# Performance work log

Measured on AMD Instinct MI355X. Metric: run time of the kernel, lower is better.

Reference implementation:

```python
import jax, jax.numpy as jnp
import numpy as np

MARGIN = 0.5
ALPHA = 1.0
BETA = 0.5
TEMP = 0.07
TEMP_MIN = 0.01
TEMP_MAX = 0.5
STEP = 1  # step_count after first forward (buffer starts at 0, incremented before use)
WARMUP = 1000


def _l2norm(x):
    return x / jnp.maximum(jnp.linalg.norm(x, axis=1, keepdims=True), 1e-12)


def _adaptive_temp(std):
    return jnp.clip(TEMP * (1.0 + std), TEMP_MIN, TEMP_MAX)


def setup_inputs() -> dict:
    key = jax.random.key(0)
    k1, k2, k3, k4, k5 = jax.random.split(key, 5)
    B, D, C, P = 4096, 1024, 1000, 2000
    return {
        "features": jax.random.normal(k1, (B, D), dtype=jnp.float32),
        "cur_proto": jax.random.normal(k2, (C, D), dtype=jnp.float32),
        "prev_proto": jax.random.normal(k3, (P, D), dtype=jnp.float32),
        "labels": jax.random.randint(k4, (B,), 0, C, dtype=jnp.int32),
        "prev_proto_labels": jax.random.randint(k5, (P,), 0, C, dtype=jnp.int32),
    }


def reference(features, cur_proto, prev_proto, labels, prev_proto_labels):
    # With randn protos, proto norms ~ sqrt(D)=32 in (1e-3, 100), so valid_mask
    # is all-True; the per-sample torch loop vectorizes exactly.
    f = _l2norm(features)          # [B, D]
    cp = _l2norm(cur_proto)        # [C, D]

    # --- positive alignment: cosine_embedding_loss(target=1) = mean(1 - cos) ---
    pos_cos = jnp.sum(f * cp[labels], axis=1)       # [B]
    pos_loss = jnp.mean(1.0 - pos_cos)

    # --- curriculum weight at step 1 ---
    w = 0.1 + 0.9 * (STEP / WARMUP)
    curr_beta = BETA * w

    # --- intra-domain InfoNCE vs current prototypes (smooth_loss branch) ---
    # all_sims per sample is a permutation of the full row of sims -> std invariant
    sims = f @ cp.T                                  # [B, C]
    std = jnp.std(sims, axis=1, ddof=1)              # torch.std is unbiased
    temp = _adaptive_temp(std)[:, None]              # [B, 1]
    logits = sims / temp
    pos_logit = jnp.take_along_axis(logits, labels[:, None], axis=1)[:, 0]
    infonce = jax.scipy.special.logsumexp(logits, axis=1) - pos_logit
    loss_neg_total = jnp.mean(infonce)

    # --- cross-domain vs previous-domain prototypes of different class ---
    pp = _l2norm(prev_proto)                         # [P, D]
    csims = f @ pp.T                                 # [B, P]
    m = (prev_proto_labels[None, :] != labels[:, None]).astype(f.dtype)  # [B, P]
    n = jnp.sum(m, axis=1)                           # [B], >1 w.h.p.
    mean = jnp.sum(csims * m, axis=1) / n
    var = jnp.sum(m * (csims - mean[:, None]) ** 2, axis=1) / (n - 1.0)
    ctemp = (_adaptive_temp(jnp.sqrt(var)) * 2.0)[:, None]
    clogits = jnp.where(m > 0, csims / ctemp, -jnp.inf)
    cross = jax.scipy.special.logsumexp(clogits, axis=1)  # [B]
    loss_neg_total = loss_neg_total + 0.3 * jnp.mean(cross)

    total = ALPHA * pos_loss + curr_beta * loss_neg_total
    return total
```

## Files before the change

kernel.cpp:

```cpp
#include <hip/hip_runtime.h>
#include <hip/hip_bf16.h>
#include <math.h>

typedef __attribute__((ext_vector_type(4))) float floatx4;
typedef __attribute__((ext_vector_type(8))) __bf16 bf16x8;

#define B_ROWS 4096
#define D_DIM  1024
#define C_CUR  1000
#define P_PREV 2000
#define C_PAD  1024
#define P_PAD  2048
#define N_TOT  (C_PAD + P_PAD)

#define LDS_BARRIER() asm volatile("s_waitcnt lgkmcnt(0)\n\ts_barrier" ::: "memory")

__device__ __forceinline__ float wave_sum(float v) {
#pragma unroll
  for (int o = 32; o > 0; o >>= 1) v += __shfl_xor(v, o, 64);
  return v;
}
__device__ __forceinline__ float wave_max(float v) {
#pragma unroll
  for (int o = 32; o > 0; o >>= 1) v = fmaxf(v, __shfl_xor(v, o, 64));
  return v;
}

__device__ __forceinline__ unsigned char f32_to_e4m3(float x) {
  unsigned u = __float_as_uint(x);
  unsigned s = (u >> 24) & 0x80u;
  float a = fabsf(x);
  if (a < 0.015625f) {
    int q = (int)rintf(a * 512.0f);
    return (unsigned char)(s | (unsigned)q);
  }
  unsigned au = u & 0x7fffffffu;
  unsigned r = au + 0x0007ffffu + ((au >> 20) & 1u);
  int e = (int)(r >> 23) - 127;
  unsigned m = (r >> 20) & 7u;
  return (unsigned char)(s | ((unsigned)(e + 7) << 3) | m);
}

__global__ __launch_bounds__(256) void norm_all_kernel(
    const float* __restrict__ features, const float* __restrict__ cur_proto,
    const float* __restrict__ prev_proto, unsigned char* __restrict__ fn,
    unsigned char* __restrict__ proto) {
  const int wv = threadIdx.x >> 6, lane = threadIdx.x & 63;
  const int r = blockIdx.x * 4 + wv;
  const float* src;
  unsigned char* dst;
  bool valid;
  if (r < B_ROWS) {
    src = features + (size_t)r * D_DIM;
    dst = fn + (size_t)r * D_DIM;
    valid = true;
  } else if (r < B_ROWS + C_PAD) {
    const int rr = r - B_ROWS;
    src = cur_proto + (size_t)rr * D_DIM;
    dst = proto + (size_t)rr * D_DIM;
    valid = rr < C_CUR;
  } else {
    const int rr = r - B_ROWS - C_PAD;
    src = prev_proto + (size_t)rr * D_DIM;
    dst = proto + (size_t)(C_PAD + rr) * D_DIM;
    valid = rr < P_PREV;
  }
  if (!valid) {
    uint4 z = {0, 0, 0, 0};
    *(uint4*)(dst + lane * 16) = z;
    return;
  }
  float4 v[4];
  float ss = 0.f;
#pragma unroll
  for (int k = 0; k < 4; ++k) {
    v[k] = *(const float4*)(src + lane * 16 + k * 4);
    ss += v[k].x * v[k].x + v[k].y * v[k].y + v[k].z * v[k].z + v[k].w * v[k].w;
  }
  ss = wave_sum(ss);
  const float inv = 1.0f / fmaxf(sqrtf(ss), 1e-12f);
  union { unsigned char b[16]; uint4 q; } o;
#pragma unroll
  for (int k = 0; k < 4; ++k) {
    o.b[k * 4 + 0] = f32_to_e4m3(v[k].x * inv);
    o.b[k * 4 + 1] = f32_to_e4m3(v[k].y * inv);
    o.b[k * 4 + 2] = f32_to_e4m3(v[k].z * inv);
    o.b[k * 4 + 3] = f32_to_e4m3(v[k].w * inv);
  }
  *(uint4*)(dst + lane * 16) = o.q;
}

#define TM    128
#define BK    32
#define LSTRB 48
#define KITER (D_DIM / BK)

__global__ __launch_bounds__(256) void gemm_fp8_kernel(
    const unsigned char* __restrict__ A,
    const unsigned char* __restrict__ Bm,
    __hip_bfloat16* __restrict__ Cm) {
  __shared__ alignas(16) unsigned char lA[2][TM * LSTRB];
  __shared__ alignas(16) unsigned char lB[2][TM * LSTRB];
  const int t = threadIdx.x;
  const int bm = blockIdx.y, bn = blockIdx.x;
  const unsigned char* Ag = A + (size_t)bm * TM * D_DIM;
  const unsigned char* Bg = Bm + (size_t)bn * TM * D_DIM;

  const int lane = t & 63, wv = t >> 6;
  const int wm = (wv >> 1) * 64, wn = (wv & 1) * 64;
  const int quad = lane >> 4, l16 = lane & 15;

  const int srow = t >> 1, shalf = (t & 1) * 16;
  const unsigned char* ap = Ag + (size_t)srow * D_DIM + shalf;
  const unsigned char* bp = Bg + (size_t)srow * D_DIM + shalf;
  const int wroff = srow * LSTRB + shalf;

  floatx4 acc[4][4] = {};

  float4 a0 = *(const float4*)(ap);
  float4 b0 = *(const float4*)(bp);
  *(float4*)(lA[0] + wroff) = a0;
  *(float4*)(lB[0] + wroff) = b0;
  a0 = *(const float4*)(ap + BK);
  b0 = *(const float4*)(bp + BK);
  LDS_BARRIER();

#pragma unroll 2
  for (int i = 0; i < KITER; ++i) {
    const int p = i & 1;
    if (i < KITER - 1) {
      *(float4*)(lA[1 - p] + wroff) = a0;
      *(float4*)(lB[1 - p] + wroff) = b0;
      const int nk = (i + 2 < KITER) ? (i + 2) * BK : (KITER - 1) * BK;
      a0 = *(const float4*)(ap + nk);
      b0 = *(const float4*)(bp + nk);
    }
    long long af[4], bfr[4];
#pragma unroll
    for (int x = 0; x < 4; ++x)
      af[x] = *(const long long*)(lA[p] + (wm + x * 16 + l16) * LSTRB + quad * 8);
#pragma unroll
    for (int y = 0; y < 4; ++y)
      bfr[y] = *(const long long*)(lB[p] + (wn + y * 16 + l16) * LSTRB + quad * 8);
#pragma unroll
    for (int x = 0; x < 4; ++x)
#pragma unroll
      for (int y = 0; y < 4; ++y)
        acc[x][y] = __builtin_amdgcn_mfma_f32_16x16x32_fp8_fp8(af[x], bfr[y], acc[x][y], 0, 0, 0);
    LDS_BARRIER();
  }

  unsigned short* Cu = (unsigned short*)Cm;
#pragma unroll
  for (int x = 0; x < 4; ++x)
#pragma unroll
    for (int y = 0; y < 4; ++y)
#pragma unroll
      for (int r = 0; r < 4; ++r) {
        const int row = bm * TM + wm + x * 16 + quad * 4 + r;
        const int col = bn * TM + wn + y * 16 + l16;
        __hip_bfloat16 h = __float2bfloat16(acc[x][y][r]);
        Cu[(size_t)row * N_TOT + col] = *(unsigned short*)&h;
      }
}

__global__ __launch_bounds__(256) void row_reduce_kernel(
    const __hip_bfloat16* __restrict__ sims, const int* __restrict__ labels,
    const int* __restrict__ ppl,
    float* __restrict__ pos_o, float* __restrict__ inf_o, float* __restrict__ crs_o) {
  const int wv = threadIdx.x >> 6, lane = threadIdx.x & 63;
  const int b = blockIdx.x * 4 + wv;
  const unsigned short* row = (const unsigned short*)sims + (size_t)b * N_TOT;
  const int lab = labels[b];

  {
    const int i1 = 512 + lane * 8;
    float vi[16];
    bf16x8 u0 = *(const bf16x8*)(row + lane * 8);
    bf16x8 u1 = *(const bf16x8*)(row + i1);
#pragma unroll
    for (int j = 0; j < 8; ++j) { vi[j] = (float)u0[j]; vi[8 + j] = (float)u1[j]; }
    float sum = 0.f, sq = 0.f, mx = -1e30f;
#pragma unroll
    for (int j = 0; j < 8; ++j) {
      float v = vi[j];
      sum += v; sq += v * v; mx = fmaxf(mx, v);
    }
#pragma unroll
    for (int j = 0; j < 8; ++j) {
      if (i1 + j < C_CUR) { float v = vi[8 + j]; sum += v; sq += v * v; mx = fmaxf(mx, v); }
    }
    sum = wave_sum(sum); sq = wave_sum(sq); mx = wave_max(mx);
    const float var = (sq - sum * sum / (float)C_CUR) / (float)(C_CUR - 1);
    const float sd = sqrtf(fmaxf(var, 0.f));
    const float temp = fminf(fmaxf(0.07f * (1.f + sd), 0.01f), 0.5f);
    const float it = 1.f / temp;
    float se = 0.f;
#pragma unroll
    for (int j = 0; j < 8; ++j) se += __expf((vi[j] - mx) * it);
#pragma unroll
    for (int j = 0; j < 8; ++j)
      if (i1 + j < C_CUR) se += __expf((vi[8 + j] - mx) * it);
    se = wave_sum(se);
    if (lane == 0) {
      __hip_bfloat16 hs;
      *(unsigned short*)&hs = row[lab];
      const float slab = __bfloat162float(hs);
      pos_o[b] = 1.f - slab;
      inf_o[b] = mx * it + logf(se) - slab * it;
    }
  }

  {
    const unsigned short* crow = row + C_PAD;
    float vc[32];
    unsigned mask = 0;
    float sum = 0.f, sq = 0.f, mx = -1e30f;
    int cnt = 0;
#pragma unroll
    for (int k = 0; k < 4; ++k) {
      const int base = k * 512 + lane * 8;
      bf16x8 u = *(const bf16x8*)(crow + base);
#pragma unroll
      for (int j = 0; j < 8; ++j) vc[k * 8 + j] = (float)u[j];
      if (base < P_PREV) {
        int4 p0 = *(const int4*)(ppl + base);
        int4 p1 = *(const int4*)(ppl + base + 4);
        const int pl[8] = {p0.x, p0.y, p0.z, p0.w, p1.x, p1.y, p1.z, p1.w};
#pragma unroll
        for (int j = 0; j < 8; ++j) {
          if (pl[j] != lab) {
            mask |= 1u << (k * 8 + j);
            float v = vc[k * 8 + j];
            sum += v; sq += v * v; mx = fmaxf(mx, v); ++cnt;
          }
        }
      }
    }
    sum = wave_sum(sum); sq = wave_sum(sq); mx = wave_max(mx);
    const float n = wave_sum((float)cnt);
    const float var = (sq - sum * sum / n) / (n - 1.f);
    const float sd = sqrtf(fmaxf(var, 0.f));
    const float ct = 2.f * fminf(fmaxf(0.07f * (1.f + sd), 0.01f), 0.5f);
    const float it = 1.f / ct;
    float se = 0.f;
#pragma unroll
    for (int e = 0; e < 32; ++e)
      if ((mask >> e) & 1u) se += __expf((vc[e] - mx) * it);
    se = wave_sum(se);
    if (lane == 0) crs_o[b] = mx * it + logf(se);
  }
}

__global__ __launch_bounds__(1024) void final_reduce_kernel(
    const float* __restrict__ pos_o, const float* __restrict__ inf_o,
    const float* __restrict__ crs_o, float* __restrict__ out) {
  const int t = threadIdx.x;
  __shared__ float sA[1024], sB[1024], sC[1024];
  float a = 0.f, bb = 0.f, c = 0.f;
  for (int i = t; i < B_ROWS; i += 1024) {
    a += pos_o[i]; bb += inf_o[i]; c += crs_o[i];
  }
  sA[t] = a; sB[t] = bb; sC[t] = c;
  __syncthreads();
  for (int o = 512; o > 0; o >>= 1) {
    if (t < o) { sA[t] += sA[t + o]; sB[t] += sB[t + o]; sC[t] += sC[t + o]; }
    __syncthreads();
  }
  if (t == 0) {
    const float invB = 1.f / (float)B_ROWS;
    const float pos = sA[0] * invB;
    const float neg = sB[0] * invB + 0.3f * sC[0] * invB;
    const float curr_beta = 0.5f * (0.1f + 0.9f * (1.0f / 1000.0f));
    out[0] = pos + curr_beta * neg;
  }
}

extern "C" void kernel_launch(void* const* d_in, const int* in_sizes, int n_in,
                              void* d_out, int out_size, void* d_ws, size_t ws_size,
                              hipStream_t stream) {
  const float* features   = (const float*)d_in[0];
  const float* cur_proto  = (const float*)d_in[1];
  const float* prev_proto = (const float*)d_in[2];
  const int*   labels     = (const int*)d_in[3];
  const int*   ppl        = (const int*)d_in[4];

  char* w = (char*)d_ws;
  unsigned char* fn    = (unsigned char*)w;
  unsigned char* proto = (unsigned char*)(w + (size_t)4 * 1024 * 1024);
  __hip_bfloat16* sims = (__hip_bfloat16*)(w + (size_t)8 * 1024 * 1024);
  char* tail = w + (size_t)8 * 1024 * 1024 + (size_t)B_ROWS * N_TOT * 2;
  float* pos_o = (float*)tail;
  float* inf_o = pos_o + B_ROWS;
  float* crs_o = inf_o + B_ROWS;

  norm_all_kernel<<<(B_ROWS + C_PAD + P_PAD) / 4, 256, 0, stream>>>(
      features, cur_proto, prev_proto, fn, proto);

  dim3 grid(N_TOT / TM, B_ROWS / TM);
  gemm_fp8_kernel<<<grid, 256, 0, stream>>>(fn, proto, sims);

  row_reduce_kernel<<<B_ROWS / 4, 256, 0, stream>>>(sims, labels, ppl, pos_o, inf_o, crs_o);
  final_reduce_kernel<<<1, 1024, 0, stream>>>(pos_o, inf_o, crs_o, (float*)d_out);
}
```

Baseline: 123.0 us.

## Remap GEMM tiles for XCD locality and deepen global prefetch to two stages

Switches the GEMM to a 1D grid and remaps block IDs so that blocks landing on the same XCD (round-robin by 8) cover contiguous row tiles that share a column tile, aiming to improve L2 reuse of the proto operand. It also manually unrolls the K loop by two, keeping two register prefetch sets in flight so global loads run two tiles ahead of compute. The cost is more live registers, which may reduce occupancy.

```diff
diff --git a/kernel.cpp b/kernel.cpp
--- a/kernel.cpp
+++ b/kernel.cpp
@@ -102,7 +102,9 @@
   __shared__ alignas(16) unsigned char lA[2][TM * LSTRB];
   __shared__ alignas(16) unsigned char lB[2][TM * LSTRB];
   const int t = threadIdx.x;
-  const int bm = blockIdx.y, bn = blockIdx.x;
+  const int l = blockIdx.x;
+  const int bm = (l & 7) * 4 + ((l >> 3) & 3);
+  const int bn = l >> 5;
   const unsigned char* Ag = A + (size_t)bm * TM * D_DIM;
   const unsigned char* Bg = Bm + (size_t)bn * TM * D_DIM;
 
@@ -117,36 +119,61 @@
 
   floatx4 acc[4][4] = {};
 
-  float4 a0 = *(const float4*)(ap);
-  float4 b0 = *(const float4*)(bp);
-  *(float4*)(lA[0] + wroff) = a0;
-  *(float4*)(lB[0] + wroff) = b0;
-  a0 = *(const float4*)(ap + BK);
-  b0 = *(const float4*)(bp + BK);
+  float4 t0a = *(const float4*)(ap);
+  float4 t0b = *(const float4*)(bp);
+  *(float4*)(lA[0] + wroff) = t0a;
+  *(float4*)(lB[0] + wroff) = t0b;
+  float4 rAa = *(const float4*)(ap + BK);
+  float4 rAb = *(const float4*)(bp + BK);
+  float4 rBa = *(const float4*)(ap + 2 * BK);
+  float4 rBb = *(const float4*)(bp + 2 * BK);
   LDS_BARRIER();
 
-#pragma unroll 2
-  for (int i = 0; i < KITER; ++i) {
-    const int p = i & 1;
-    if (i < KITER - 1) {
-      *(float4*)(lA[1 - p] + wroff) = a0;
-      *(float4*)(lB[1 - p] + wroff) = b0;
-      const int nk = (i + 2 < KITER) ? (i + 2) * BK : (KITER - 1) * BK;
-      a0 = *(const float4*)(ap + nk);
-      b0 = *(const float4*)(bp + nk);
-    }
-    long long af[4], bfr[4];
-#pragma unroll
-    for (int x = 0; x < 4; ++x)
-      af[x] = *(const long long*)(lA[p] + (wm + x * 16 + l16) * LSTRB + quad * 8);
-#pragma unroll
-    for (int y = 0; y < 4; ++y)
-      bfr[y] = *(const long long*)(lB[p] + (wn + y * 16 + l16) * LSTRB + quad * 8);
-#pragma unroll
-    for (int x = 0; x < 4; ++x)
+  for (int j = 0; j < KITER; j += 2) {
+    if (j < KITER - 1) {
+      *(float4*)(lA[1] + wroff) = rAa;
+      *(float4*)(lB[1] + wroff) = rAb;
+      const int nk = (j + 3 < KITER ? j + 3 : KITER - 1) * BK;
+      rAa = *(const float4*)(ap + nk);
+      rAb = *(const float4*)(bp + nk);
+    }
+    {
+      long long af[4], bfr[4];
+#pragma unroll
+      for (int x = 0; x < 4; ++x)
+        af[x] = *(const long long*)(lA[0] + (wm + x * 16 + l16) * LSTRB + quad * 8);
 #pragma unroll
       for (int y = 0; y < 4; ++y)
-        acc[x][y] = __builtin_amdgcn_mfma_f32_16x16x32_fp8_fp8(af[x], bfr[y], acc[x][y], 0, 0, 0);
+        bfr[y] = *(const long long*)(lB[0] + (wn + y * 16 + l16) * LSTRB + quad * 8);
+#pragma unroll
+      for (int x = 0; x < 4; ++x)
+#pragma unroll
+        for (int y = 0; y < 4; ++y)
+          acc[x][y] = __builtin_amdgcn_mfma_f32_16x16x32_fp8_fp8(af[x], bfr[y], acc[x][y], 0, 0, 0);
+    }
+    LDS_BARRIER();
+
+    if (j + 1 < KITER - 1) {
+      *(float4*)(lA[0] + wroff) = rBa;
+      *(float4*)(lB[0] + wroff) = rBb;
+      const int nk = (j + 4 < KITER ? j + 4 : KITER - 1) * BK;
+      rBa = *(const float4*)(ap + nk);
+      rBb = *(const float4*)(bp + nk);
+    }
+    {
+      long long af[4], bfr[4];
+#pragma unroll
+      for (int x = 0; x < 4; ++x)
+        af[x] = *(const long long*)(lA[1] + (wm + x * 16 + l16) * LSTRB + quad * 8);
+#pragma unroll
+      for (int y = 0; y < 4; ++y)
+        bfr[y] = *(const long long*)(lB[1] + (wn + y * 16 + l16) * LSTRB + quad * 8);
+#pragma unroll
+      for (int x = 0; x < 4; ++x)
+#pragma unroll
+        for (int y = 0; y < 4; ++y)
+          acc[x][y] = __builtin_amdgcn_mfma_f32_16x16x32_fp8_fp8(af[x], bfr[y], acc[x][y], 0, 0, 0);
+    }
     LDS_BARRIER();
   }
 
@@ -297,8 +324,7 @@
   norm_all_kernel<<<(B_ROWS + C_PAD + P_PAD) / 4, 256, 0, stream>>>(
       features, cur_proto, prev_proto, fn, proto);
 
-  dim3 grid(N_TOT / TM, B_ROWS / TM);
-  gemm_fp8_kernel<<<grid, 256, 0, stream>>>(fn, proto, sims);
+  gemm_fp8_kernel<<<(N_TOT / TM) * (B_ROWS / TM), 256, 0, stream>>>(fn, proto, sims);
 
   row_reduce_kernel<<<B_ROWS / 4, 256, 0, stream>>>(sims, labels, ppl, pos_o, inf_o, crs_o);
   final_reduce_kernel<<<1, 1024, 0, stream>>>(pos_o, inf_o, crs_o, (float*)d_out);
```

Result: no change. 124.6 us (+1.4%).
